# Kernel optimization log

Hardware: AMD Instinct MI355X
Metric: run time of the kernel (lower is better)

The kernel has to match this reference:

```python
import jax, jax.numpy as jnp
import numpy as np

DN = ('NCHW', 'OIHW', 'NCHW')

def _conv(x, w, pad):
    return jax.lax.conv_general_dilated(x, w, window_strides=(1, 1),
                                        padding=[(pad, pad), (pad, pad)],
                                        dimension_numbers=DN)

def _channel_shuffle(x, perm):
    # x: [B, C, H, W]; perm: [C, H*W] per-channel spatial permutation
    B, C, H, W = x.shape
    y = jnp.take_along_axis(x.reshape(B, C, H * W), perm[None, :, :], axis=2)
    return y.reshape(B, C, H, W)

def setup_inputs() -> dict:
    key = jax.random.key(0)
    k = jax.random.split(key, 6)
    B, Cin, H, W = 32, 1024, 28, 28
    P1, P2, P3 = 256, 256, 1024
    HW = H * W
    x = jax.random.normal(k[0], (B, Cin, H, W), dtype=jnp.float32)
    w1 = jax.random.normal(k[1], (P1, Cin, 1, 1), dtype=jnp.float32) * np.sqrt(2.0 / Cin)
    wd = jax.random.normal(k[2], (P2, P1, 3, 3), dtype=jnp.float32) * np.sqrt(2.0 / (P1 * 9))
    w3 = jax.random.normal(k[3], (P3, P2, 1, 1), dtype=jnp.float32) * np.sqrt(2.0 / P2)
    perm_dconv = jax.vmap(lambda kk: jax.random.permutation(kk, HW))(
        jax.random.split(k[4], P1)).astype(jnp.int32)
    perm_res = jax.vmap(lambda kk: jax.random.permutation(kk, HW))(
        jax.random.split(k[5], Cin)).astype(jnp.int32)
    return {"x": x, "w1": w1, "wd": wd, "w3": w3,
            "perm_dconv": perm_dconv, "perm_res": perm_res}

def reference(x, w1, wd, w3, perm_dconv, perm_res):
    # conv1 (1x1) + relu
    y = jax.nn.relu(_conv(x, w1, 0))
    # Dconv_shuffle: per-channel spatial shuffle then 3x3 conv (pad=1), relu
    y = _channel_shuffle(y, perm_dconv)
    y = jax.nn.relu(_conv(y, wd, 1))
    # conv3 (1x1)
    y = _conv(y, w3, 0)
    # residual: per-channel spatially shuffled input, add, relu
    res = _channel_shuffle(x, perm_res)
    return jax.nn.relu(y + res)
```

## Files before the change

kernel.cpp:

```cpp
#include <hip/hip_runtime.h>
#include <hip/hip_bf16.h>

#define BATCH 32
#define CIN   1024
#define HW    784
#define WIMG  28
#define PADW  30
#define PADHW 900
#define P1    256
#define P2    256
#define P3    1024
#define NFLAT (BATCH * HW)

typedef __attribute__((ext_vector_type(8))) short bfrag_t;
typedef __attribute__((ext_vector_type(8))) unsigned short usvec8;
typedef __attribute__((ext_vector_type(4))) unsigned short usvec4;
typedef __attribute__((ext_vector_type(4))) float accvec_t;

static __device__ __forceinline__ unsigned short f2bf(float f) {
    union { __hip_bfloat16 h; unsigned short u; } cv;
    cv.h = __float2bfloat16(f);
    return cv.u;
}
static __device__ __forceinline__ float bf2f(unsigned short u) {
    union { float f; unsigned int i; } cv;
    cv.i = ((unsigned int)u) << 16;
    return cv.f;
}

#define GLDS16(g, l) __builtin_amdgcn_global_load_lds(                      \
        (const __attribute__((address_space(1))) void*)(g),                 \
        (__attribute__((address_space(3))) void*)(l), 16, 0, 0)

__global__ __launch_bounds__(256) void permT_kernel(const int* __restrict__ perm,
                                                    int* __restrict__ permT) {
    int p = blockIdx.x, c = threadIdx.x;
    permT[p * P1 + c] = perm[c * HW + p];
}

__global__ __launch_bounds__(256) void pack_weights_kernel(
        const float* __restrict__ w1, const float* __restrict__ wd,
        const float* __restrict__ w3, unsigned short* __restrict__ w1b,
        unsigned short* __restrict__ wdb, unsigned short* __restrict__ w3b) {
    int i = blockIdx.x * 256 + threadIdx.x;
    if (i < 262144) w1b[i] = f2bf(w1[i]);
    int i2 = i - 262144;
    if (i2 >= 0 && i2 < 262144) w3b[i2] = f2bf(w3[i2]);
    int i3 = i - 524288;
    if (i3 >= 0 && i3 < 589824) {
        int m = i3 / 2304, rem = i3 - m * 2304;
        int k = rem / 9, r = rem - k * 9;
        wdb[((size_t)r * P2 + m) * P1 + k] = f2bf(wd[i3]);
    }
}

__global__ __launch_bounds__(256) void transpose_x_kernel(const float* __restrict__ x,
                                                          unsigned short* __restrict__ xt) {
    __shared__ __align__(16) unsigned short T[64 * 72];
    const int c0 = blockIdx.x * 64;
    const int n0 = blockIdx.y * 64;
    const int t  = threadIdx.x;
    const int f  = t & 15;
    const int cg = t >> 4;
    const int n  = n0 + f * 4;
    const int b  = n / HW, hw = n - b * HW;
    const float* xb = x + ((size_t)b * CIN + c0 + cg * 4) * HW + hw;
    float4 v0 = *(const float4*)&xb[0];
    float4 v1 = *(const float4*)&xb[HW];
    float4 v2 = *(const float4*)&xb[2 * HW];
    float4 v3 = *(const float4*)&xb[3 * HW];
    const float* vr[4] = {(const float*)&v0, (const float*)&v1,
                          (const float*)&v2, (const float*)&v3};
#pragma unroll
    for (int q = 0; q < 4; ++q) {
        usvec4 w;
        w[0] = f2bf(vr[0][q]);
        w[1] = f2bf(vr[1][q]);
        w[2] = f2bf(vr[2][q]);
        w[3] = f2bf(vr[3][q]);
        *(usvec4*)&T[(f * 4 + q) * 72 + cg * 4] = w;
    }
    __syncthreads();
#pragma unroll
    for (int it = 0; it < 2; ++it) {
        int idx  = it * 256 + t;
        int hw_l = idx >> 3, cgo = idx & 7;
        usvec8 w = *(const usvec8*)&T[hw_l * 72 + cgo * 8];
        *(usvec8*)&xt[(size_t)(n0 + hw_l) * CIN + c0 + cgo * 8] = w;
    }
}

__global__ __launch_bounds__(256) void res_shuffle_kernel(const float* __restrict__ x,
                                                          const int* __restrict__ perm_res,
                                                          unsigned short* __restrict__ res) {
    __shared__ float Lx[8 * 788];
    const int g0 = blockIdx.x * 8;
    const int t = threadIdx.x;
#pragma unroll
    for (int it = 0; it < 7; ++it) {
        int chunk = it * 256 + t;
        if (chunk < 1568) {
            int r = chunk / 196, off = (chunk - r * 196) * 4;
            float4 v = *(const float4*)&x[(size_t)(g0 + r) * HW + off];
            *(float4*)&Lx[r * 788 + off] = v;
        }
    }
    __syncthreads();
    const int q0 = t & 63;
#pragma unroll
    for (int rp = 0; rp < 2; ++rp) {
        int r = rp * 4 + (t >> 6);
        int g = g0 + r;
        int m = g & (CIN - 1);
        const int* pr = perm_res + (size_t)m * HW;
#pragma unroll
        for (int it = 0; it < 13; ++it) {
            int q = it * 64 + q0;
            if (q < HW) {
                int pv = pr[q];
                res[(size_t)g * HW + q] = f2bf(Lx[r * 788 + pv]);
            }
        }
    }
}

__global__ __launch_bounds__(256) void shuffle_pad_kernel(const unsigned short* __restrict__ y1c,
                                                          const int* __restrict__ permT,
                                                          unsigned short* __restrict__ y1sp) {
    __shared__ unsigned short Ly[32 * 800];
    const int b  = blockIdx.x >> 3;
    const int c0 = (blockIdx.x & 7) * 32;
    const int t = threadIdx.x;
#pragma unroll
    for (int it = 0; it < 13; ++it) {
        int chunk = it * 256 + t;
        if (chunk < 3136) {
            int c = chunk / 98, off8 = (chunk - c * 98) * 8;
            usvec8 v = *(const usvec8*)&y1c[((size_t)(b * P1 + c0 + c)) * HW + off8];
            *(usvec8*)&Ly[c * 800 + off8] = v;
        }
    }
    __syncthreads();
    const int pc = t & 31, pi = t >> 5;
    unsigned short* yb = y1sp + (size_t)b * PADHW * P1 + c0 + pc;
#pragma unroll 4
    for (int it = 0; it < 98; ++it) {
        int p = it * 8 + pi;
        int pv = permT[p * P1 + c0 + pc];
        unsigned short val = Ly[pc * 800 + pv];
        int ph = p / WIMG, pw = p - ph * WIMG;
        yb[(size_t)((ph + 1) * PADW + pw + 1) * P1] = val;
    }
}


__global__ __launch_bounds__(256) void conv1_kernel(const unsigned short* __restrict__ xt,
                                                    const unsigned short* __restrict__ w1b,
                                                    unsigned short* __restrict__ y1c) {
    __shared__ __align__(16) unsigned short As[128 * 64];
    __shared__ __align__(16) unsigned short Bs[128 * 64];
    const int m0 = blockIdx.x * 128;
    const int n0 = blockIdx.y * 128;
    const int t = threadIdx.x;
    const int lane = t & 63, wave = t >> 6;
    const int l15 = lane & 15, quad = lane >> 4;
    const int wm = wave & 1, wn = wave >> 1;
    const int grow = lane >> 3;
    const int gsw  = ((lane & 7) ^ grow) << 3;
    const unsigned short* Asrc[4];
    const unsigned short* Bsrc[4];
    int ldso[4];
#pragma unroll
    for (int j = 0; j < 4; ++j) {
        int q = wave * 4 + j;
        int row = (q << 3) + grow;
        Asrc[j] = w1b + (size_t)(m0 + row) * CIN + gsw;
        Bsrc[j] = xt + (size_t)(n0 + row) * CIN + gsw;
        ldso[j] = q * 512;
    }
    const int coff0 = ((quad)     ^ (l15 & 7)) << 3;
    const int coff1 = ((quad + 4) ^ (l15 & 7)) << 3;

    accvec_t acc[4][4];
    const accvec_t zero = {0.f, 0.f, 0.f, 0.f};
#pragma unroll
    for (int i = 0; i < 4; ++i)
#pragma unroll
        for (int j = 0; j < 4; ++j) acc[i][j] = zero;

    for (int k0 = 0; k0 < CIN; k0 += 64) {
#pragma unroll
        for (int j = 0; j < 4; ++j) {
            GLDS16(Asrc[j] + k0, &As[ldso[j]]);
            GLDS16(Bsrc[j] + k0, &Bs[ldso[j]]);
        }
        __syncthreads();
        bfrag_t af[4], bfr[4];
#pragma unroll
        for (int i = 0; i < 4; ++i) {
            af[i]  = *(const bfrag_t*)&As[(wm * 64 + i * 16 + l15) * 64 + coff0];
            bfr[i] = *(const bfrag_t*)&Bs[(wn * 64 + i * 16 + l15) * 64 + coff0];
        }
#pragma unroll
        for (int im = 0; im < 4; ++im)
#pragma unroll
            for (int in = 0; in < 4; ++in)
                acc[im][in] = __builtin_amdgcn_mfma_f32_16x16x32_bf16(af[im], bfr[in], acc[im][in], 0, 0, 0);
#pragma unroll
        for (int i = 0; i < 4; ++i) {
            af[i]  = *(const bfrag_t*)&As[(wm * 64 + i * 16 + l15) * 64 + coff1];
            bfr[i] = *(const bfrag_t*)&Bs[(wn * 64 + i * 16 + l15) * 64 + coff1];
        }
#pragma unroll
        for (int im = 0; im < 4; ++im)
#pragma unroll
            for (int in = 0; in < 4; ++in)
                acc[im][in] = __builtin_amdgcn_mfma_f32_16x16x32_bf16(af[im], bfr[in], acc[im][in], 0, 0, 0);
        __syncthreads();
    }
#pragma unroll
    for (int in = 0; in < 4; ++in) {
        const int n = n0 + wn * 64 + in * 16 + l15;
        const int b = n / HW, hw = n - b * HW;
#pragma unroll
        for (int im = 0; im < 4; ++im) {
#pragma unroll
            for (int r = 0; r < 4; ++r) {
                const int m = m0 + wm * 64 + im * 16 + (quad << 2) + r;
                float v = acc[im][in][r];
                v = v > 0.f ? v : 0.f;
                y1c[((size_t)(b * P1 + m)) * HW + hw] = f2bf(v);
            }
        }
    }
}

__global__ __launch_bounds__(256) void dconv_kernel(const unsigned short* __restrict__ y1sp,
                                                    const unsigned short* __restrict__ wdb,
                                                    unsigned short* __restrict__ y2t) {
    __shared__ __align__(16) unsigned short As[128 * 64];
    __shared__ __align__(16) unsigned short Bs[128 * 64];
    const int m0 = blockIdx.x * 128;
    const int n0 = blockIdx.y * 128;
    const int t = threadIdx.x;
    const int lane = t & 63, wave = t >> 6;
    const int l15 = lane & 15, quad = lane >> 4;
    const int wm = wave & 1, wn = wave >> 1;
    const int grow = lane >> 3;
    const int gsw  = ((lane & 7) ^ grow) << 3;
    const unsigned short* Asrc[4];
    const unsigned short* Bsrc[4];
    int ldso[4];
#pragma unroll
    for (int j = 0; j < 4; ++j) {
        int q = wave * 4 + j;
        int row = (q << 3) + grow;
        Asrc[j] = wdb + (size_t)(m0 + row) * P1 + gsw;
        int n = n0 + row;
        int b = n / HW, hw = n - b * HW;
        int h = hw / WIMG, w = hw - h * WIMG;
        Bsrc[j] = y1sp + ((size_t)b * PADHW + h * PADW + w) * P1 + gsw;
        ldso[j] = q * 512;
    }
    const int coff0 = ((quad)     ^ (l15 & 7)) << 3;
    const int coff1 = ((quad + 4) ^ (l15 & 7)) << 3;

    accvec_t acc[4][4];
    const accvec_t zero = {0.f, 0.f, 0.f, 0.f};
#pragma unroll
    for (int i = 0; i < 4; ++i)
#pragma unroll
        for (int j = 0; j < 4; ++j) acc[i][j] = zero;

    for (int r = 0; r < 9; ++r) {
        const int kh = r / 3, kw = r - kh * 3;
        const size_t aoff = (size_t)r * (P1 * P2);
        const int taboff = (kh * PADW + kw) * P1;
        for (int k0 = 0; k0 < P1; k0 += 64) {
#pragma unroll
            for (int j = 0; j < 4; ++j) {
                GLDS16(Asrc[j] + aoff + k0, &As[ldso[j]]);
                GLDS16(Bsrc[j] + taboff + k0, &Bs[ldso[j]]);
            }
            __syncthreads();
            bfrag_t af[4], bfr[4];
#pragma unroll
            for (int i = 0; i < 4; ++i) {
                af[i]  = *(const bfrag_t*)&As[(wm * 64 + i * 16 + l15) * 64 + coff0];
                bfr[i] = *(const bfrag_t*)&Bs[(wn * 64 + i * 16 + l15) * 64 + coff0];
            }
#pragma unroll
            for (int im = 0; im < 4; ++im)
#pragma unroll
                for (int in = 0; in < 4; ++in)
                    acc[im][in] = __builtin_amdgcn_mfma_f32_16x16x32_bf16(bfr[in], af[im], acc[im][in], 0, 0, 0);
#pragma unroll
            for (int i = 0; i < 4; ++i) {
                af[i]  = *(const bfrag_t*)&As[(wm * 64 + i * 16 + l15) * 64 + coff1];
                bfr[i] = *(const bfrag_t*)&Bs[(wn * 64 + i * 16 + l15) * 64 + coff1];
            }
#pragma unroll
            for (int im = 0; im < 4; ++im)
#pragma unroll
                for (int in = 0; in < 4; ++in)
                    acc[im][in] = __builtin_amdgcn_mfma_f32_16x16x32_bf16(bfr[in], af[im], acc[im][in], 0, 0, 0);
            __syncthreads();
        }
    }
#pragma unroll
    for (int im = 0; im < 4; ++im) {
        const int m = m0 + wm * 64 + im * 16 + l15;
#pragma unroll
        for (int in = 0; in < 4; ++in) {
#pragma unroll
            for (int r = 0; r < 4; ++r) {
                const int n = n0 + wn * 64 + in * 16 + (quad << 2) + r;
                float v = acc[im][in][r];
                v = v > 0.f ? v : 0.f;
                y2t[(size_t)n * P2 + m] = f2bf(v);
            }
        }
    }
}

__global__ __launch_bounds__(256) void conv3_kernel(const unsigned short* __restrict__ y2t,
                                                    const unsigned short* __restrict__ w3b,
                                                    const unsigned short* __restrict__ res,
                                                    float* __restrict__ out) {
    __shared__ __align__(16) unsigned short SMEM[8448];
    unsigned short* As = SMEM;
    unsigned short* Bs = SMEM + 4096;
    float* Obuf = (float*)SMEM;

    const int m0 = blockIdx.x * 128;
    const int n0 = blockIdx.y * 128;
    const int t = threadIdx.x;
    const int lane = t & 63, wave = t >> 6;
    const int l15 = lane & 15, quad = lane >> 4;
    const int wm = wave & 1, wn = wave >> 1;
    const int srow = lane >> 2, c8 = (lane & 3) << 3;
    const int row0 = wave * 32 + srow, row1 = row0 + 16;

    const unsigned short* a0 = w3b + (size_t)(m0 + row0) * P2 + c8;
    const unsigned short* a1 = w3b + (size_t)(m0 + row1) * P2 + c8;
    const unsigned short* b0 = y2t + (size_t)(n0 + row0) * P2 + c8;
    const unsigned short* b1 = y2t + (size_t)(n0 + row1) * P2 + c8;
    unsigned short* Ad0 = &As[(wave * 2 + 0) * 512];
    unsigned short* Ad1 = &As[(wave * 2 + 1) * 512];
    unsigned short* Bd0 = &Bs[(wave * 2 + 0) * 512];
    unsigned short* Bd1 = &Bs[(wave * 2 + 1) * 512];

    const int erow = t >> 3, eseg = t & 7;
    const int n_e  = n0 + eseg * 16;
    const int b_e  = n_e / HW;
    const int hw_e = n_e - b_e * HW;
    const size_t ebase0 = ((size_t)(b_e * P3 + m0 + erow)) * HW + hw_e;

    usvec8 rsA = *(const usvec8*)&res[ebase0];
    usvec8 rsB = *(const usvec8*)&res[ebase0 + 8];

    accvec_t acc[4][4];
    const accvec_t zero = {0.f, 0.f, 0.f, 0.f};
#pragma unroll
    for (int i = 0; i < 4; ++i)
#pragma unroll
        for (int j = 0; j < 4; ++j) acc[i][j] = zero;

    for (int k0 = 0; k0 < P2; k0 += 32) {
        GLDS16(a0 + k0, Ad0);
        GLDS16(a1 + k0, Ad1);
        GLDS16(b0 + k0, Bd0);
        GLDS16(b1 + k0, Bd1);
        __syncthreads();
        bfrag_t af[4], bfr[4];
#pragma unroll
        for (int i = 0; i < 4; ++i) {
            af[i]  = *(const bfrag_t*)&As[(wm * 64 + i * 16 + l15) * 32 + (quad << 3)];
            bfr[i] = *(const bfrag_t*)&Bs[(wn * 64 + i * 16 + l15) * 32 + (quad << 3)];
        }
#pragma unroll
        for (int im = 0; im < 4; ++im)
#pragma unroll
            for (int in = 0; in < 4; ++in)
                acc[im][in] = __builtin_amdgcn_mfma_f32_16x16x32_bf16(af[im], bfr[in], acc[im][in], 0, 0, 0);
        __syncthreads();
    }

#pragma unroll
    for (int c = 0; c < 4; ++c) {
        if (wm == (c >> 1)) {
            const int imb = (c & 1) * 2;
#pragma unroll
            for (int i2 = 0; i2 < 2; ++i2)
#pragma unroll
                for (int in = 0; in < 4; ++in)
#pragma unroll
                    for (int r = 0; r < 4; ++r)
                        Obuf[(i2 * 16 + (quad << 2) + r) * 132 + wn * 64 + in * 16 + l15] =
                            acc[imb + i2][in][r];
        }
        __syncthreads();
        usvec8 nxA = rsA, nxB = rsB;
        if (c < 3) {
            const size_t nb = ebase0 + (size_t)(c + 1) * 32 * HW;
            nxA = *(const usvec8*)&res[nb];
            nxB = *(const usvec8*)&res[nb + 8];
        }
        {
            const size_t base = ebase0 + (size_t)c * 32 * HW;
            float ov[16];
#pragma unroll
            for (int q4 = 0; q4 < 4; ++q4) {
                float4 v = *(const float4*)&Obuf[erow * 132 + eseg * 16 + q4 * 4];
                ov[q4 * 4 + 0] = v.x; ov[q4 * 4 + 1] = v.y;
                ov[q4 * 4 + 2] = v.z; ov[q4 * 4 + 3] = v.w;
            }
#pragma unroll
            for (int q4 = 0; q4 < 4; ++q4) {
                float4 w;
                float e0, e1, e2, e3;
                const int j = q4 * 4;
                e0 = ov[j + 0] + bf2f((unsigned short)(j + 0 < 8 ? rsA[j + 0] : rsB[j + 0 - 8]));
                e1 = ov[j + 1] + bf2f((unsigned short)(j + 1 < 8 ? rsA[j + 1] : rsB[j + 1 - 8]));
                e2 = ov[j + 2] + bf2f((unsigned short)(j + 2 < 8 ? rsA[j + 2] : rsB[j + 2 - 8]));
                e3 = ov[j + 3] + bf2f((unsigned short)(j + 3 < 8 ? rsA[j + 3] : rsB[j + 3 - 8]));
                w.x = e0 > 0.f ? e0 : 0.f;
                w.y = e1 > 0.f ? e1 : 0.f;
                w.z = e2 > 0.f ? e2 : 0.f;
                w.w = e3 > 0.f ? e3 : 0.f;
                *(float4*)&out[base + q4 * 4] = w;
            }
        }
        rsA = nxA; rsB = nxB;
        if (c < 3) __syncthreads();
    }
}

extern "C" void kernel_launch(void* const* d_in, const int* in_sizes, int n_in,
                              void* d_out, int out_size, void* d_ws, size_t ws_size,
                              hipStream_t stream) {
    const float* x      = (const float*)d_in[0];
    const float* w1     = (const float*)d_in[1];
    const float* wd     = (const float*)d_in[2];
    const float* w3     = (const float*)d_in[3];
    const int*   perm_d = (const int*)d_in[4];
    const int*   perm_r = (const int*)d_in[5];
    float*       out    = (float*)d_out;

    char* ws = (char*)d_ws;
    unsigned short* y1sp  = (unsigned short*)(ws + 0);
    unsigned short* y2t   = (unsigned short*)(ws + 14745600);
    int*            permT = (int*)(ws + 27590656);
    unsigned short* w1b   = (unsigned short*)(ws + 28393472);
    unsigned short* wdb   = (unsigned short*)(ws + 28917760);
    unsigned short* w3b   = (unsigned short*)(ws + 30097408);
    unsigned short* xt    = (unsigned short*)(ws + 30621696);
    unsigned short* resb  = xt;
    unsigned short* y1c   = y2t;

    hipMemsetAsync(y1sp, 0, (size_t)BATCH * PADHW * P1 * sizeof(unsigned short), stream);
    permT_kernel<<<dim3(HW), dim3(256), 0, stream>>>(perm_d, permT);
    pack_weights_kernel<<<dim3(4352), dim3(256), 0, stream>>>(w1, wd, w3, w1b, wdb, w3b);
    transpose_x_kernel<<<dim3(CIN / 64, NFLAT / 64), dim3(256), 0, stream>>>(x, xt);

    conv1_kernel<<<dim3(P1 / 128, NFLAT / 128), dim3(256), 0, stream>>>(xt, w1b, y1c);
    res_shuffle_kernel<<<dim3(BATCH * CIN / 8), dim3(256), 0, stream>>>(x, perm_r, resb);
    shuffle_pad_kernel<<<dim3(BATCH * 8), dim3(256), 0, stream>>>(y1c, permT, y1sp);
    dconv_kernel<<<dim3(P2 / 128, NFLAT / 128), dim3(256), 0, stream>>>(y1sp, wdb, y2t);
    conv3_kernel<<<dim3(P3 / 128, NFLAT / 128), dim3(256), 0, stream>>>(y2t, w3b, resb, out);
}
```

Before: 355.5 us.

## Double-buffer LDS tiles in conv1, dconv and conv3 GEMM main loops

Converts the three MFMA GEMM kernels from single-buffered LDS staging into a two-stage ping-pong pipeline. Global-to-LDS loads for the next K slice are issued before computing on the current buffer, with explicit vmcnt waits and raw s_barrier calls in place of __syncthreads. The aim is to overlap global memory latency with MFMA work. In exchange, LDS use per block doubles, which may reduce occupancy, and correctness depends on the hand-tuned waitcnt counts.

Result: no change. 356.5 us (+0.3%).

```diff
diff --git a/kernel.cpp b/kernel.cpp
--- a/kernel.cpp
+++ b/kernel.cpp
@@ -31,6 +31,16 @@
 #define GLDS16(g, l) __builtin_amdgcn_global_load_lds(                      \
         (const __attribute__((address_space(1))) void*)(g),                 \
         (__attribute__((address_space(3))) void*)(l), 16, 0, 0)
+
+#define RAW_BARRIER() do {                         \
+        __builtin_amdgcn_sched_barrier(0);         \
+        __builtin_amdgcn_s_barrier();              \
+        __builtin_amdgcn_sched_barrier(0);         \
+    } while (0)
+#define WAITCNT_VM(N) do {                                        \
+        asm volatile("s_waitcnt vmcnt(" #N ")" ::: "memory");     \
+        __builtin_amdgcn_sched_barrier(0);                        \
+    } while (0)
 
 __global__ __launch_bounds__(256) void permT_kernel(const int* __restrict__ perm,
                                                     int* __restrict__ permT) {
@@ -157,8 +167,8 @@
 __global__ __launch_bounds__(256) void conv1_kernel(const unsigned short* __restrict__ xt,
                                                     const unsigned short* __restrict__ w1b,
                                                     unsigned short* __restrict__ y1c) {
-    __shared__ __align__(16) unsigned short As[128 * 64];
-    __shared__ __align__(16) unsigned short Bs[128 * 64];
+    __shared__ __align__(16) unsigned short As[2 * 128 * 64];
+    __shared__ __align__(16) unsigned short Bs[2 * 128 * 64];
     const int m0 = blockIdx.x * 128;
     const int n0 = blockIdx.y * 128;
     const int t = threadIdx.x;
@@ -188,18 +198,23 @@
 #pragma unroll
         for (int j = 0; j < 4; ++j) acc[i][j] = zero;
 
-    for (int k0 = 0; k0 < CIN; k0 += 64) {
+    auto stage = [&](int cur, int k0) {
+        unsigned short* Ab = As + cur * 8192;
+        unsigned short* Bb = Bs + cur * 8192;
 #pragma unroll
         for (int j = 0; j < 4; ++j) {
-            GLDS16(Asrc[j] + k0, &As[ldso[j]]);
-            GLDS16(Bsrc[j] + k0, &Bs[ldso[j]]);
-        }
-        __syncthreads();
+            GLDS16(Asrc[j] + k0, Ab + ldso[j]);
+            GLDS16(Bsrc[j] + k0, Bb + ldso[j]);
+        }
+    };
+    auto compute = [&](int cur) {
+        const unsigned short* Ab = As + cur * 8192;
+        const unsigned short* Bb = Bs + cur * 8192;
         bfrag_t af[4], bfr[4];
 #pragma unroll
         for (int i = 0; i < 4; ++i) {
-            af[i]  = *(const bfrag_t*)&As[(wm * 64 + i * 16 + l15) * 64 + coff0];
-            bfr[i] = *(const bfrag_t*)&Bs[(wn * 64 + i * 16 + l15) * 64 + coff0];
+            af[i]  = *(const bfrag_t*)&Ab[(wm * 64 + i * 16 + l15) * 64 + coff0];
+            bfr[i] = *(const bfrag_t*)&Bb[(wn * 64 + i * 16 + l15) * 64 + coff0];
         }
 #pragma unroll
         for (int im = 0; im < 4; ++im)
@@ -208,15 +223,28 @@
                 acc[im][in] = __builtin_amdgcn_mfma_f32_16x16x32_bf16(af[im], bfr[in], acc[im][in], 0, 0, 0);
 #pragma unroll
         for (int i = 0; i < 4; ++i) {
-            af[i]  = *(const bfrag_t*)&As[(wm * 64 + i * 16 + l15) * 64 + coff1];
-            bfr[i] = *(const bfrag_t*)&Bs[(wn * 64 + i * 16 + l15) * 64 + coff1];
+            af[i]  = *(const bfrag_t*)&Ab[(wm * 64 + i * 16 + l15) * 64 + coff1];
+            bfr[i] = *(const bfrag_t*)&Bb[(wn * 64 + i * 16 + l15) * 64 + coff1];
         }
 #pragma unroll
         for (int im = 0; im < 4; ++im)
 #pragma unroll
             for (int in = 0; in < 4; ++in)
                 acc[im][in] = __builtin_amdgcn_mfma_f32_16x16x32_bf16(af[im], bfr[in], acc[im][in], 0, 0, 0);
-        __syncthreads();
+    };
+
+    stage(0, 0);
+    for (int s = 0; s < 16; s += 2) {
+        stage(1, (s + 1) << 6);
+        WAITCNT_VM(8);
+        RAW_BARRIER();
+        compute(0);
+        RAW_BARRIER();
+        if (s + 2 < 16) { stage(0, (s + 2) << 6); WAITCNT_VM(8); }
+        else            { WAITCNT_VM(0); }
+        RAW_BARRIER();
+        compute(1);
+        RAW_BARRIER();
     }
 #pragma unroll
     for (int in = 0; in < 4; ++in) {
@@ -238,8 +266,8 @@
 __global__ __launch_bounds__(256) void dconv_kernel(const unsigned short* __restrict__ y1sp,
                                                     const unsigned short* __restrict__ wdb,
                                                     unsigned short* __restrict__ y2t) {
-    __shared__ __align__(16) unsigned short As[128 * 64];
-    __shared__ __align__(16) unsigned short Bs[128 * 64];
+    __shared__ __align__(16) unsigned short As[2 * 128 * 64];
+    __shared__ __align__(16) unsigned short Bs[2 * 128 * 64];
     const int m0 = blockIdx.x * 128;
     const int n0 = blockIdx.y * 128;
     const int t = threadIdx.x;
@@ -272,40 +300,58 @@
 #pragma unroll
         for (int j = 0; j < 4; ++j) acc[i][j] = zero;
 
-    for (int r = 0; r < 9; ++r) {
+    auto stage = [&](int cur, int s) {
+        const int r  = s >> 2;
+        const int k0 = (s & 3) << 6;
         const int kh = r / 3, kw = r - kh * 3;
-        const size_t aoff = (size_t)r * (P1 * P2);
-        const int taboff = (kh * PADW + kw) * P1;
-        for (int k0 = 0; k0 < P1; k0 += 64) {
-#pragma unroll
-            for (int j = 0; j < 4; ++j) {
-                GLDS16(Asrc[j] + aoff + k0, &As[ldso[j]]);
-                GLDS16(Bsrc[j] + taboff + k0, &Bs[ldso[j]]);
-            }
-            __syncthreads();
-            bfrag_t af[4], bfr[4];
-#pragma unroll
-            for (int i = 0; i < 4; ++i) {
-                af[i]  = *(const bfrag_t*)&As[(wm * 64 + i * 16 + l15) * 64 + coff0];
-                bfr[i] = *(const bfrag_t*)&Bs[(wn * 64 + i * 16 + l15) * 64 + coff0];
-            }
-#pragma unroll
-            for (int im = 0; im < 4; ++im)
-#pragma unroll
-                for (int in = 0; in < 4; ++in)
-                    acc[im][in] = __builtin_amdgcn_mfma_f32_16x16x32_bf16(bfr[in], af[im], acc[im][in], 0, 0, 0);
-#pragma unroll
-            for (int i = 0; i < 4; ++i) {
-                af[i]  = *(const bfrag_t*)&As[(wm * 64 + i * 16 + l15) * 64 + coff1];
-                bfr[i] = *(const bfrag_t*)&Bs[(wn * 64 + i * 16 + l15) * 64 + coff1];
-            }
-#pragma unroll
-            for (int im = 0; im < 4; ++im)
-#pragma unroll
-                for (int in = 0; in < 4; ++in)
-                    acc[im][in] = __builtin_amdgcn_mfma_f32_16x16x32_bf16(bfr[in], af[im], acc[im][in], 0, 0, 0);
-            __syncthreads();
-        }
+        const size_t aoff = (size_t)r * (P1 * P2) + k0;
+        const int    toff = (kh * PADW + kw) * P1 + k0;
+        unsigned short* Ab = As + cur * 8192;
+        unsigned short* Bb = Bs + cur * 8192;
+#pragma unroll
+        for (int j = 0; j < 4; ++j) {
+            GLDS16(Asrc[j] + aoff, Ab + ldso[j]);
+            GLDS16(Bsrc[j] + toff, Bb + ldso[j]);
+        }
+    };
+    auto compute = [&](int cur) {
+        const unsigned short* Ab = As + cur * 8192;
+        const unsigned short* Bb = Bs + cur * 8192;
+        bfrag_t af[4], bfr[4];
+#pragma unroll
+        for (int i = 0; i < 4; ++i) {
+            af[i]  = *(const bfrag_t*)&Ab[(wm * 64 + i * 16 + l15) * 64 + coff0];
+            bfr[i] = *(const bfrag_t*)&Bb[(wn * 64 + i * 16 + l15) * 64 + coff0];
+        }
+#pragma unroll
+        for (int im = 0; im < 4; ++im)
+#pragma unroll
+            for (int in = 0; in < 4; ++in)
+                acc[im][in] = __builtin_amdgcn_mfma_f32_16x16x32_bf16(bfr[in], af[im], acc[im][in], 0, 0, 0);
+#pragma unroll
+        for (int i = 0; i < 4; ++i) {
+            af[i]  = *(const bfrag_t*)&Ab[(wm * 64 + i * 16 + l15) * 64 + coff1];
+            bfr[i] = *(const bfrag_t*)&Bb[(wn * 64 + i * 16 + l15) * 64 + coff1];
+        }
+#pragma unroll
+        for (int im = 0; im < 4; ++im)
+#pragma unroll
+            for (int in = 0; in < 4; ++in)
+                acc[im][in] = __builtin_amdgcn_mfma_f32_16x16x32_bf16(bfr[in], af[im], acc[im][in], 0, 0, 0);
+    };
+
+    stage(0, 0);
+    for (int s = 0; s < 36; s += 2) {
+        stage(1, s + 1);
+        WAITCNT_VM(8);
+        RAW_BARRIER();
+        compute(0);
+        RAW_BARRIER();
+        if (s + 2 < 36) { stage(0, s + 2); WAITCNT_VM(8); }
+        else            { WAITCNT_VM(0); }
+        RAW_BARRIER();
+        compute(1);
+        RAW_BARRIER();
     }
 #pragma unroll
     for (int im = 0; im < 4; ++im) {
@@ -327,9 +373,9 @@
                                                     const unsigned short* __restrict__ w3b,
                                                     const unsigned short* __restrict__ res,
                                                     float* __restrict__ out) {
-    __shared__ __align__(16) unsigned short SMEM[8448];
-    unsigned short* As = SMEM;
-    unsigned short* Bs = SMEM + 4096;
+    __shared__ __align__(16) unsigned short SMEM[16384];
+    unsigned short* AsB = SMEM;
+    unsigned short* BsB = SMEM + 8192;
     float* Obuf = (float*)SMEM;
 
     const int m0 = blockIdx.x * 128;
@@ -345,10 +391,7 @@
     const unsigned short* a1 = w3b + (size_t)(m0 + row1) * P2 + c8;
     const unsigned short* b0 = y2t + (size_t)(n0 + row0) * P2 + c8;
     const unsigned short* b1 = y2t + (size_t)(n0 + row1) * P2 + c8;
-    unsigned short* Ad0 = &As[(wave * 2 + 0) * 512];
-    unsigned short* Ad1 = &As[(wave * 2 + 1) * 512];
-    unsigned short* Bd0 = &Bs[(wave * 2 + 0) * 512];
-    unsigned short* Bd1 = &Bs[(wave * 2 + 1) * 512];
+    const int o0 = (wave * 2 + 0) * 512, o1 = (wave * 2 + 1) * 512;
 
     const int erow = t >> 3, eseg = t & 7;
     const int n_e  = n0 + eseg * 16;
@@ -366,24 +409,42 @@
 #pragma unroll
         for (int j = 0; j < 4; ++j) acc[i][j] = zero;
 
-    for (int k0 = 0; k0 < P2; k0 += 32) {
-        GLDS16(a0 + k0, Ad0);
-        GLDS16(a1 + k0, Ad1);
-        GLDS16(b0 + k0, Bd0);
-        GLDS16(b1 + k0, Bd1);
-        __syncthreads();
+    auto stage = [&](int cur, int k0) {
+        unsigned short* Ab = AsB + cur * 4096;
+        unsigned short* Bb = BsB + cur * 4096;
+        GLDS16(a0 + k0, Ab + o0);
+        GLDS16(a1 + k0, Ab + o1);
+        GLDS16(b0 + k0, Bb + o0);
+        GLDS16(b1 + k0, Bb + o1);
+    };
+    auto compute = [&](int cur) {
+        const unsigned short* Ab = AsB + cur * 4096;
+        const unsigned short* Bb = BsB + cur * 4096;
         bfrag_t af[4], bfr[4];
 #pragma unroll
         for (int i = 0; i < 4; ++i) {
-            af[i]  = *(const bfrag_t*)&As[(wm * 64 + i * 16 + l15) * 32 + (quad << 3)];
-            bfr[i] = *(const bfrag_t*)&Bs[(wn * 64 + i * 16 + l15) * 32 + (quad << 3)];
+            af[i]  = *(const bfrag_t*)&Ab[(wm * 64 + i * 16 + l15) * 32 + (quad << 3)];
+            bfr[i] = *(const bfrag_t*)&Bb[(wn * 64 + i * 16 + l15) * 32 + (quad << 3)];
         }
 #pragma unroll
         for (int im = 0; im < 4; ++im)
 #pragma unroll
             for (int in = 0; in < 4; ++in)
                 acc[im][in] = __builtin_amdgcn_mfma_f32_16x16x32_bf16(af[im], bfr[in], acc[im][in], 0, 0, 0);
-        __syncthreads();
+    };
+
+    stage(0, 0);
+    for (int s = 0; s < 8; s += 2) {
+        stage(1, (s + 1) << 5);
+        WAITCNT_VM(4);
+        RAW_BARRIER();
+        compute(0);
+        RAW_BARRIER();
+        if (s + 2 < 8) { stage(0, (s + 2) << 5); WAITCNT_VM(4); }
+        else           { WAITCNT_VM(0); }
+        RAW_BARRIER();
+        compute(1);
+        RAW_BARRIER();
     }
 
 #pragma unroll
```
